# Optimization experiments

Measured on AMD Instinct MI355X. Metric: run time of the kernel, lower is better.

Reference implementation:

```python
import jax, jax.numpy as jnp
import numpy as np

N_HEADS = 16
N_UNITS = 1024
D_K = N_UNITS // N_HEADS
B, S = 2, 2048


def setup_inputs() -> dict:
    key = jax.random.key(0)
    ks = jax.random.split(key, 12)
    bound = 1.0 / np.sqrt(N_UNITS)
    u = lambda k, shape: jax.random.uniform(k, shape, jnp.float32, -bound, bound)
    inp = {
        'query': jax.random.normal(ks[0], (B, S, N_UNITS), jnp.float32),
        'key_': jax.random.normal(ks[1], (B, S, N_UNITS), jnp.float32),
        'value': jax.random.normal(ks[2], (B, S, N_UNITS), jnp.float32),
        'mask': jnp.broadcast_to(jnp.tril(jnp.ones((S, S), jnp.int32)), (B, S, S)),
        'Wq': u(ks[3], (N_UNITS, N_UNITS)), 'bq': u(ks[4], (N_UNITS,)),
        'Wk': u(ks[5], (N_UNITS, N_UNITS)), 'bk': u(ks[6], (N_UNITS,)),
        'Wv': u(ks[7], (N_UNITS, N_UNITS)), 'bv': u(ks[8], (N_UNITS,)),
        'Wo': u(ks[9], (N_UNITS, N_UNITS)), 'bo': u(ks[10], (N_UNITS,)),
    }
    return inp


def _split_heads(x):
    # [B,S,U] -> [B,H,S,Dk]
    b, s, _ = x.shape
    return x.reshape(b, s, N_HEADS, D_K).transpose(0, 2, 1, 3)


def reference(query, key_, value, mask, Wq, bq, Wk, bk, Wv, bv, Wo, bo):
    q = _split_heads(query @ Wq.T + bq)
    k = _split_heads(key_ @ Wk.T + bk)
    v = _split_heads(value @ Wv.T + bv)
    scores = jnp.einsum('bhqd,bhkd->bhqk', q, k) / jnp.sqrt(jnp.float32(D_K))
    scores = jnp.where(mask[:, None, :, :] == 0, jnp.float32(-1e10), scores)
    attn = jax.nn.softmax(scores, axis=-1)  # dropout omitted (eval / p=0)
    A = jnp.einsum('bhqk,bhkd->bhqd', attn, v)
    A = A.transpose(0, 2, 1, 3).reshape(query.shape[0], -1, N_UNITS)
    return A @ Wo.T + bo
```

## Files before the change

### kernel.cpp

```cpp
#include <hip/hip_runtime.h>
#include <hip/hip_bf16.h>

#define U     1024
#define SLEN  2048
#define HEADS 16
#define DK    64
#define MTOT  4096
#define MU    (MTOT * U)
#define UU    (U * U)

#define QSCALE2 0.18033688f

typedef unsigned short u16;
typedef short bf16x8 __attribute__((ext_vector_type(8)));
typedef u16 u16x4 __attribute__((ext_vector_type(4)));
typedef float f32x4 __attribute__((ext_vector_type(4)));

__device__ __forceinline__ u16 f2bf(float x) {
  union { float f; unsigned int u; } v; v.f = x;
  unsigned int r = v.u + 0x7fffu + ((v.u >> 16) & 1u);
  return (u16)(r >> 16);
}
__device__ __forceinline__ u16 f2bf_rz(float x) {
  return (u16)(__builtin_bit_cast(unsigned int, x) >> 16);
}

#if __has_builtin(__builtin_amdgcn_exp2f)
__device__ __forceinline__ float exp2_fast(float x) { return __builtin_amdgcn_exp2f(x); }
#else
__device__ __forceinline__ float exp2_fast(float x) { return __expf(x * 0.6931472f); }
#endif

__device__ __forceinline__ void async16(const u16* g, u16* lds) {
  __builtin_amdgcn_global_load_lds((const __attribute__((address_space(1))) void*)g,
                                   (__attribute__((address_space(3))) void*)lds,
                                   16, 0, 0);
}

#define DPP_F(x, ctrl) __builtin_bit_cast(float, \
    __builtin_amdgcn_update_dpp(0, __builtin_bit_cast(int, (x)), (ctrl), 0xF, 0xF, true))

__device__ __forceinline__ float rsum16(float x) {
  x += DPP_F(x, 0xB1);
  x += DPP_F(x, 0x4E);
  x += DPP_F(x, 0x141);
  x += DPP_F(x, 0x140);
  return x;
}

__global__ __launch_bounds__(256) void convert_kernel(
    const float* __restrict__ q, const float* __restrict__ k, const float* __restrict__ v,
    const float* __restrict__ wq, const float* __restrict__ wk,
    const float* __restrict__ wv, const float* __restrict__ wo,
    u16* __restrict__ cq, u16* __restrict__ ck, u16* __restrict__ cv,
    u16* __restrict__ cwq, u16* __restrict__ cwk, u16* __restrict__ cwv,
    u16* __restrict__ cwo) {
  const int t = blockIdx.y;
  const float* src = (t == 0) ? q : (t == 1) ? k : (t == 2) ? v
                   : (t == 3) ? wq : (t == 4) ? wk : (t == 5) ? wv : wo;
  u16* dst = (t == 0) ? cq : (t == 1) ? ck : (t == 2) ? cv
           : (t == 3) ? cwq : (t == 4) ? cwk : (t == 5) ? cwv : cwo;
  const int n4 = ((t < 3) ? MU : UU) >> 2;
  const int stride = gridDim.x * blockDim.x;
  for (int i = blockIdx.x * blockDim.x + threadIdx.x; i < n4; i += stride) {
    float4 f = ((const float4*)src)[i];
    u16x4 o = {f2bf(f.x), f2bf(f.y), f2bf(f.z), f2bf(f.w)};
    ((u16x4*)dst)[i] = o;
  }
}

__device__ __forceinline__ void stage_tile(const u16* __restrict__ src, int kt,
                                           u16* lds, int tid) {
#pragma unroll
  for (int c = 0; c < 2; ++c) {
    int f = c * 256 + tid;
    int row = f >> 2;
    int qs = f & 3;
    int q = qs ^ ((row >> 1) & 3);
    const u16* g = src + (size_t)row * U + kt + q * 8;
    u16* l = lds + (size_t)(f & ~63) * 8;
    async16(g, l);
  }
}

__device__ __forceinline__ bf16x8 read_frag(const u16* lds, int lrow, int quad) {
  int qs = quad ^ ((lrow >> 1) & 3);
  return *(const bf16x8*)(lds + (size_t)(lrow * 4 + qs) * 8);
}

__device__ __forceinline__ void gemm128(const u16* __restrict__ X,
                                        const u16* __restrict__ W,
                                        int m0, int n0, int tid,
                                        u16* lds,
                                        f32x4 acc[4][4]) {
  const int l = tid & 63, w = tid >> 6;
  const int quad = l >> 4, l15 = l & 15;
  const int wm = w & 1, wn = w >> 1;
  const u16* Xb = X + (size_t)m0 * U;
  const u16* Wb = W + (size_t)n0 * U;

  stage_tile(Xb, 0, lds, tid);
  stage_tile(Wb, 0, lds + 4096, tid);

  int bufsel = 0;
  for (int kt = 0; kt < U; kt += 32) {
    const int nxt = (bufsel == 2) ? 0 : bufsel + 1;
    if (kt + 32 < U) {
      stage_tile(Xb, kt + 32, lds + nxt * 8192, tid);
      stage_tile(Wb, kt + 32, lds + nxt * 8192 + 4096, tid);
      __builtin_amdgcn_sched_barrier(0);
      asm volatile("s_waitcnt vmcnt(4)" ::: "memory");
    } else {
      __builtin_amdgcn_sched_barrier(0);
      asm volatile("s_waitcnt vmcnt(0)" ::: "memory");
    }
    __builtin_amdgcn_sched_barrier(0);
    __builtin_amdgcn_s_barrier();
    __builtin_amdgcn_sched_barrier(0);

    const u16* la = lds + bufsel * 8192;
    const u16* lb = la + 4096;
    bf16x8 af[4], bfm[4];
#pragma unroll
    for (int i = 0; i < 4; ++i) af[i] = read_frag(la, wm * 64 + i * 16 + l15, quad);
#pragma unroll
    for (int t = 0; t < 4; ++t) bfm[t] = read_frag(lb, wn * 64 + t * 16 + l15, quad);
#pragma unroll
    for (int i = 0; i < 4; ++i)
#pragma unroll
      for (int t = 0; t < 4; ++t)
        acc[i][t] = __builtin_amdgcn_mfma_f32_16x16x32_bf16(af[i], bfm[t], acc[i][t], 0, 0, 0);
    bufsel = nxt;
  }
}

__device__ __forceinline__ void xcd_remap(int* m0, int* n0) {
  const int id = blockIdx.x + (blockIdx.y << 3);
  const int k = id & 7, j = id >> 3;
  const int xp = j >> 2;
  const int yp = (k << 2) | (j & 3);
  *m0 = yp * 128;
  *n0 = xp * 128;
}

__global__ __launch_bounds__(256) void qkv_gemm(
    const u16* __restrict__ q_in, const u16* __restrict__ k_in, const u16* __restrict__ v_in,
    const u16* __restrict__ Wq, const u16* __restrict__ Wk, const u16* __restrict__ Wv,
    const float* __restrict__ bq, const float* __restrict__ bk, const float* __restrict__ bv,
    u16* __restrict__ q_ws, u16* __restrict__ k_ws, u16* __restrict__ v_ws) {
  __shared__ __align__(16) u16 lds3[3 * 8192];
  const int z = blockIdx.z;
  const u16* X = (z == 0) ? q_in : (z == 1) ? k_in : v_in;
  const u16* W = (z == 0) ? Wq : (z == 1) ? Wk : Wv;
  const float* bias = (z == 0) ? bq : (z == 1) ? bk : bv;
  int m0, n0;
  xcd_remap(&m0, &n0);
  const int tid = threadIdx.x;
  f32x4 acc[4][4];
#pragma unroll
  for (int i = 0; i < 4; ++i)
#pragma unroll
    for (int t = 0; t < 4; ++t) acc[i][t] = (f32x4){0.f, 0.f, 0.f, 0.f};
  gemm128(X, W, m0, n0, tid, lds3, acc);

  const int l = tid & 63, w = tid >> 6;
  const int quad = l >> 4, l15 = l & 15;
  const int wm = w & 1, wn = w >> 1;
  const float osc = (z == 0) ? QSCALE2 : 1.0f;
#pragma unroll
  for (int t = 0; t < 4; ++t) {
    const int n = n0 + wn * 64 + t * 16 + l15;
    const float bb = bias[n];
    const int h = n >> 6, d = n & 63;
#pragma unroll
    for (int i = 0; i < 4; ++i) {
#pragma unroll
      for (int r = 0; r < 4; ++r) {
        const int m = m0 + wm * 64 + i * 16 + quad * 4 + r;
        const int b = m >> 11, s = m & (SLEN - 1);
        const int bh = b * HEADS + h;
        const u16 ov = f2bf((acc[i][t][r] + bb) * osc);
        if (z == 0)      q_ws[((size_t)bh * SLEN + s) * DK + d] = ov;
        else if (z == 1) k_ws[((size_t)bh * SLEN + s) * DK + d] = ov;
        else             v_ws[((size_t)bh * DK + d) * SLEN + s] = ov;
      }
    }
  }
}

__global__ __launch_bounds__(256, 4) void flash_attn(const u16* __restrict__ q_ws,
                                                     const u16* __restrict__ k_ws,
                                                     const u16* __restrict__ v_ws,
                                                     u16* __restrict__ a_ws) {
  __shared__ __align__(16) u16 kbuf[2][4096];
  __shared__ __align__(16) u16 vbuf[2][4096];
  __shared__ __align__(16) u16 p_lds[4][16][72];
  const int id = blockIdx.x;
  const int bh = id & 31;
  const int qblk = 31 - (id >> 5);
  const int tid = threadIdx.x;
  const int w = tid >> 6, l = tid & 63;
  const int quad = l >> 4, l15 = l & 15;
  const int qrow = qblk * 64 + w * 16;
  const int jn = qblk;

  const u16* qb = q_ws + (size_t)bh * SLEN * DK;
  const u16* kb = k_ws + (size_t)bh * SLEN * DK;
  const u16* vb = v_ws + (size_t)bh * DK * SLEN;

  bf16x8 aq0 = *(const bf16x8*)(qb + (size_t)(qrow + l15) * DK + quad * 8);
  bf16x8 aq1 = *(const bf16x8*)(qb + (size_t)(qrow + l15) * DK + 32 + quad * 8);

  f32x4 o[4];
  float l_run[4];
#pragma unroll
  for (int t = 0; t < 4; ++t) o[t] = (f32x4){0.f, 0.f, 0.f, 0.f};
#pragma unroll
  for (int r = 0; r < 4; ++r) l_run[r] = 0.f;

  auto stage = [&](int j0, int b) {
#pragma unroll
    for (int c = 0; c < 2; ++c) {
      const int f = c * 256 + tid;
      const int row = f >> 3, qs = f & 7;
      const int q = qs ^ (row & 7);
      u16* kdst = kbuf[b] + (size_t)(f & ~63) * 8;
      u16* vdst = vbuf[b] + (size_t)(f & ~63) * 8;
      async16(kb + (size_t)(j0 + row) * DK + q * 8, kdst);
      async16(vb + (size_t)row * SLEN + j0 + q * 8, vdst);
    }
  };

  stage(0, 0);
  __syncthreads();

  for (int jt = 0; jt <= jn; ++jt) {
    const int buf = jt & 1;
    if (jt < jn) stage((jt + 1) * 64, buf ^ 1);
    const int j0 = jt * 64;
    const int swz = l15 & 7;

    float sv[4][4];
#pragma unroll
    for (int t = 0; t < 4; ++t) {
      const u16* krow = kbuf[buf] + (size_t)(t * 16 + l15) * 64;
      bf16x8 kf0 = *(const bf16x8*)(krow + ((quad ^ swz) * 8));
      bf16x8 kf1 = *(const bf16x8*)(krow + (((quad + 4) ^ swz) * 8));
      f32x4 acc = (f32x4){0.f, 0.f, 0.f, 0.f};
      acc = __builtin_amdgcn_mfma_f32_16x16x32_bf16(aq0, kf0, acc, 0, 0, 0);
      acc = __builtin_amdgcn_mfma_f32_16x16x32_bf16(aq1, kf1, acc, 0, 0, 0);
#pragma unroll
      for (int r = 0; r < 4; ++r) sv[t][r] = acc[r];
    }
    if (jt == jn) {
#pragma unroll
      for (int t = 0; t < 4; ++t) {
        const int col = j0 + t * 16 + l15;
#pragma unroll
        for (int r = 0; r < 4; ++r)
          if (col > qrow + quad * 4 + r) sv[t][r] = -1e30f;
      }
    }
#pragma unroll
    for (int t = 0; t < 4; ++t) {
#pragma unroll
      for (int r = 0; r < 4; ++r) {
        const float p = exp2_fast(sv[t][r]);
        l_run[r] += p;
        p_lds[w][quad * 4 + r][t * 16 + l15] = f2bf_rz(p);
      }
    }
    bf16x8 pa0 = *(const bf16x8*)&p_lds[w][l15][quad * 8];
    bf16x8 pa1 = *(const bf16x8*)&p_lds[w][l15][32 + quad * 8];
#pragma unroll
    for (int t = 0; t < 4; ++t) {
      const u16* vrow = vbuf[buf] + (size_t)(t * 16 + l15) * 64;
      bf16x8 vf0 = *(const bf16x8*)(vrow + ((quad ^ swz) * 8));
      bf16x8 vf1 = *(const bf16x8*)(vrow + (((quad + 4) ^ swz) * 8));
      o[t] = __builtin_amdgcn_mfma_f32_16x16x32_bf16(pa0, vf0, o[t], 0, 0, 0);
      o[t] = __builtin_amdgcn_mfma_f32_16x16x32_bf16(pa1, vf1, o[t], 0, 0, 0);
    }
    __syncthreads();
  }
  const int b = bh >> 4, h = bh & 15;
  float inv[4];
#pragma unroll
  for (int r = 0; r < 4; ++r) inv[r] = 1.f / rsum16(l_run[r]);
#pragma unroll
  for (int r = 0; r < 4; ++r) {
    const int s = qrow + quad * 4 + r;
    u16* orow = a_ws + ((size_t)b * SLEN + s) * U + h * DK;
#pragma unroll
    for (int t = 0; t < 4; ++t)
      orow[t * 16 + l15] = f2bf(o[t][r] * inv[r]);
  }
}

__global__ __launch_bounds__(256) void oproj_gemm(const u16* __restrict__ A,
                                                  const u16* __restrict__ Wo,
                                                  const float* __restrict__ bo,
                                                  float* __restrict__ out) {
  __shared__ __align__(16) u16 lds3[3 * 8192];
  int m0, n0;
  xcd_remap(&m0, &n0);
  const int tid = threadIdx.x;
  f32x4 acc[4][4];
#pragma unroll
  for (int i = 0; i < 4; ++i)
#pragma unroll
    for (int t = 0; t < 4; ++t) acc[i][t] = (f32x4){0.f, 0.f, 0.f, 0.f};
  gemm128(A, Wo, m0, n0, tid, lds3, acc);

  const int l = tid & 63, w = tid >> 6;
  const int quad = l >> 4, l15 = l & 15;
  const int wm = w & 1, wn = w >> 1;
#pragma unroll
  for (int t = 0; t < 4; ++t) {
    const int n = n0 + wn * 64 + t * 16 + l15;
    const float bb = bo[n];
#pragma unroll
    for (int i = 0; i < 4; ++i) {
#pragma unroll
      for (int r = 0; r < 4; ++r) {
        const int m = m0 + wm * 64 + i * 16 + quad * 4 + r;
        out[(size_t)m * U + n] = acc[i][t][r] + bb;
      }
    }
  }
}

extern "C" void kernel_launch(void* const* d_in, const int* in_sizes, int n_in,
                              void* d_out, int out_size, void* d_ws, size_t ws_size,
                              hipStream_t stream) {
  (void)in_sizes; (void)n_in; (void)out_size; (void)ws_size;
  const float* query = (const float*)d_in[0];
  const float* key_  = (const float*)d_in[1];
  const float* value = (const float*)d_in[2];
  const float* Wq = (const float*)d_in[4];
  const float* bq = (const float*)d_in[5];
  const float* Wk = (const float*)d_in[6];
  const float* bk = (const float*)d_in[7];
  const float* Wv = (const float*)d_in[8];
  const float* bv = (const float*)d_in[9];
  const float* Wo = (const float*)d_in[10];
  const float* bo = (const float*)d_in[11];

  u16* ws = (u16*)d_ws;
  u16* cq  = ws;
  u16* ck  = cq + MU;
  u16* cv  = ck + MU;
  u16* cwq = cv + MU;
  u16* cwk = cwq + UU;
  u16* cwv = cwk + UU;
  u16* cwo = cwv + UU;
  u16* q_ws = cwo + UU;
  u16* k_ws = q_ws + MU;
  u16* v_ws = k_ws + MU;
  u16* a_ws = v_ws + MU;
  float* out = (float*)d_out;

  convert_kernel<<<dim3(512, 7), 256, 0, stream>>>(query, key_, value, Wq, Wk, Wv, Wo,
                                                   cq, ck, cv, cwq, cwk, cwv, cwo);
  qkv_gemm<<<dim3(8, 32, 3), 256, 0, stream>>>(cq, ck, cv, cwq, cwk, cwv,
                                               bq, bk, bv, q_ws, k_ws, v_ws);
  flash_attn<<<dim3(1024), 256, 0, stream>>>(q_ws, k_ws, v_ws, a_ws);
  oproj_gemm<<<dim3(8, 32), 256, 0, stream>>>(a_ws, cwo, bo, out);
}
```

Before: 230.7 us.

## Replace QKV GEMM with 256x256-tile, 512-thread, triple-buffered kernel

The 128x128 QKV projection kernel (768 blocks of 256 threads) is replaced by a 256x256-tile kernel using 512 threads, 96KB of dynamic LDS and a three-stage async load pipeline. The MFMA work is split into two halves separated by barriers, with s_setprio raising priority during math. A custom block-to-tile mapping spreads the 192 tiles across XCDs. The larger tiles raise operand reuse and cut global traffic, at the cost of fewer blocks (192 across 256 CUs), which leaves some CUs idle and adds more register pressure.

```diff
diff --git a/kernel.cpp b/kernel.cpp
--- a/kernel.cpp
+++ b/kernel.cpp
@@ -69,6 +69,124 @@
   }
 }
 
+__device__ __forceinline__ bf16x8 read_frag(const u16* lds, int lrow, int quad) {
+  int qs = quad ^ ((lrow >> 1) & 3);
+  return *(const bf16x8*)(lds + (size_t)(lrow * 4 + qs) * 8);
+}
+
+__global__ __launch_bounds__(512, 2) void qkv_gemm256(
+    const u16* __restrict__ q_in, const u16* __restrict__ k_in, const u16* __restrict__ v_in,
+    const u16* __restrict__ Wq, const u16* __restrict__ Wk, const u16* __restrict__ Wv,
+    const float* __restrict__ bq, const float* __restrict__ bk, const float* __restrict__ bv,
+    u16* __restrict__ q_ws, u16* __restrict__ k_ws, u16* __restrict__ v_ws) {
+  extern __shared__ __align__(16) u16 lds[];
+  const int id = blockIdx.x;
+  const int k8 = id & 7, j = id >> 3;
+  const int jm = j / 3, jn = j - jm * 3;
+  const int mp = (k8 & 1) * 8 + jm;
+  const int np = (k8 >> 1) * 3 + jn;
+  const int z = np >> 2;
+  const int m0 = mp * 256, n0 = (np & 3) * 256;
+  const u16* X = (z == 0) ? q_in : (z == 1) ? k_in : v_in;
+  const u16* W = (z == 0) ? Wq : (z == 1) ? Wk : Wv;
+  const float* bias = (z == 0) ? bq : (z == 1) ? bk : bv;
+  const u16* Xb = X + (size_t)m0 * U;
+  const u16* Wb = W + (size_t)n0 * U;
+
+  const int tid = threadIdx.x;
+  const int l = tid & 63, w = tid >> 6;
+  const int quad = l >> 4, l15 = l & 15;
+  const int wm = w & 1, wn = w >> 1;
+
+  auto stage = [&](const u16* src, int kt, u16* slot) {
+#pragma unroll
+    for (int L = 0; L < 2; ++L) {
+      const int f = L * 512 + tid;
+      const int row = f >> 2, qs = f & 3;
+      const int q = qs ^ ((row >> 1) & 3);
+      async16(src + (size_t)row * U + kt + q * 8, slot + (size_t)(f & ~63) * 8);
+    }
+  };
+
+  f32x4 acc[8][4];
+#pragma unroll
+  for (int i = 0; i < 8; ++i)
+#pragma unroll
+    for (int n = 0; n < 4; ++n) acc[i][n] = (f32x4){0.f, 0.f, 0.f, 0.f};
+
+  stage(Xb, 0, lds);
+  stage(Wb, 0, lds + 8192);
+  stage(Xb, 32, lds + 16384);
+  stage(Wb, 32, lds + 16384 + 8192);
+  __builtin_amdgcn_sched_barrier(0);
+  asm volatile("s_waitcnt vmcnt(4)" ::: "memory");
+  __builtin_amdgcn_s_barrier();
+
+  int scur = 0;
+  for (int t = 0; t < 32; ++t) {
+    u16* slot = lds + scur * 16384;
+    int s2 = scur + 2; if (s2 >= 3) s2 -= 3;
+    u16* slot2 = lds + s2 * 16384;
+    const int kt2 = (t + 2) * 32;
+    bf16x8 af[4], bf[4];
+#pragma unroll
+    for (int i = 0; i < 4; ++i) af[i] = read_frag(slot, wm * 128 + i * 16 + l15, quad);
+#pragma unroll
+    for (int n = 0; n < 4; ++n) bf[n] = read_frag(slot + 8192, wn * 64 + n * 16 + l15, quad);
+    if (t < 30) stage(Xb, kt2, slot2);
+    __builtin_amdgcn_s_barrier();
+    __builtin_amdgcn_s_setprio(1);
+#pragma unroll
+    for (int i = 0; i < 4; ++i)
+#pragma unroll
+      for (int n = 0; n < 4; ++n)
+        acc[i][n] = __builtin_amdgcn_mfma_f32_16x16x32_bf16(af[i], bf[n], acc[i][n], 0, 0, 0);
+    __builtin_amdgcn_s_setprio(0);
+    __builtin_amdgcn_s_barrier();
+#pragma unroll
+    for (int i = 0; i < 4; ++i) af[i] = read_frag(slot, wm * 128 + (4 + i) * 16 + l15, quad);
+    if (t < 30) {
+      stage(Wb, kt2, slot2 + 8192);
+      __builtin_amdgcn_sched_barrier(0);
+      asm volatile("s_waitcnt vmcnt(4)" ::: "memory");
+    } else {
+      __builtin_amdgcn_sched_barrier(0);
+      asm volatile("s_waitcnt vmcnt(0)" ::: "memory");
+    }
+    __builtin_amdgcn_s_barrier();
+    __builtin_amdgcn_s_setprio(1);
+#pragma unroll
+    for (int i = 0; i < 4; ++i)
+#pragma unroll
+      for (int n = 0; n < 4; ++n)
+        acc[4 + i][n] = __builtin_amdgcn_mfma_f32_16x16x32_bf16(af[i], bf[n], acc[4 + i][n], 0, 0, 0);
+    __builtin_amdgcn_s_setprio(0);
+    __builtin_amdgcn_s_barrier();
+    scur = (scur == 2) ? 0 : scur + 1;
+  }
+
+  const float osc = (z == 0) ? QSCALE2 : 1.0f;
+#pragma unroll
+  for (int nf = 0; nf < 4; ++nf) {
+    const int n = n0 + wn * 64 + nf * 16 + l15;
+    const float bb = bias[n];
+    const int h = n >> 6, d = n & 63;
+#pragma unroll
+    for (int mi = 0; mi < 8; ++mi) {
+#pragma unroll
+      for (int r = 0; r < 4; ++r) {
+        const int m = m0 + wm * 128 + mi * 16 + quad * 4 + r;
+        const int b = m >> 11, s = m & (SLEN - 1);
+        const int bh = b * HEADS + h;
+        const u16 ov = f2bf((acc[mi][nf][r] + bb) * osc);
+        if (z == 0)      q_ws[((size_t)bh * SLEN + s) * DK + d] = ov;
+        else if (z == 1) k_ws[((size_t)bh * SLEN + s) * DK + d] = ov;
+        else             v_ws[((size_t)bh * DK + d) * SLEN + s] = ov;
+      }
+    }
+  }
+}
+
 __device__ __forceinline__ void stage_tile(const u16* __restrict__ src, int kt,
                                            u16* lds, int tid) {
 #pragma unroll
@@ -81,11 +199,6 @@
     u16* l = lds + (size_t)(f & ~63) * 8;
     async16(g, l);
   }
-}
-
-__device__ __forceinline__ bf16x8 read_frag(const u16* lds, int lrow, int quad) {
-  int qs = quad ^ ((lrow >> 1) & 3);
-  return *(const bf16x8*)(lds + (size_t)(lrow * 4 + qs) * 8);
 }
 
 __device__ __forceinline__ void gemm128(const u16* __restrict__ X,
@@ -141,51 +254,6 @@
   const int yp = (k << 2) | (j & 3);
   *m0 = yp * 128;
   *n0 = xp * 128;
-}
-
-__global__ __launch_bounds__(256) void qkv_gemm(
-    const u16* __restrict__ q_in, const u16* __restrict__ k_in, const u16* __restrict__ v_in,
-    const u16* __restrict__ Wq, const u16* __restrict__ Wk, const u16* __restrict__ Wv,
-    const float* __restrict__ bq, const float* __restrict__ bk, const float* __restrict__ bv,
-    u16* __restrict__ q_ws, u16* __restrict__ k_ws, u16* __restrict__ v_ws) {
-  __shared__ __align__(16) u16 lds3[3 * 8192];
-  const int z = blockIdx.z;
-  const u16* X = (z == 0) ? q_in : (z == 1) ? k_in : v_in;
-  const u16* W = (z == 0) ? Wq : (z == 1) ? Wk : Wv;
-  const float* bias = (z == 0) ? bq : (z == 1) ? bk : bv;
-  int m0, n0;
-  xcd_remap(&m0, &n0);
-  const int tid = threadIdx.x;
-  f32x4 acc[4][4];
-#pragma unroll
-  for (int i = 0; i < 4; ++i)
-#pragma unroll
-    for (int t = 0; t < 4; ++t) acc[i][t] = (f32x4){0.f, 0.f, 0.f, 0.f};
-  gemm128(X, W, m0, n0, tid, lds3, acc);
-
-  const int l = tid & 63, w = tid >> 6;
-  const int quad = l >> 4, l15 = l & 15;
-  const int wm = w & 1, wn = w >> 1;
-  const float osc = (z == 0) ? QSCALE2 : 1.0f;
-#pragma unroll
-  for (int t = 0; t < 4; ++t) {
-    const int n = n0 + wn * 64 + t * 16 + l15;
-    const float bb = bias[n];
-    const int h = n >> 6, d = n & 63;
-#pragma unroll
-    for (int i = 0; i < 4; ++i) {
-#pragma unroll
-      for (int r = 0; r < 4; ++r) {
-        const int m = m0 + wm * 64 + i * 16 + quad * 4 + r;
-        const int b = m >> 11, s = m & (SLEN - 1);
-        const int bh = b * HEADS + h;
-        const u16 ov = f2bf((acc[i][t][r] + bb) * osc);
-        if (z == 0)      q_ws[((size_t)bh * SLEN + s) * DK + d] = ov;
-        else if (z == 1) k_ws[((size_t)bh * SLEN + s) * DK + d] = ov;
-        else             v_ws[((size_t)bh * DK + d) * SLEN + s] = ov;
-      }
-    }
-  }
 }
 
 __global__ __launch_bounds__(256, 4) void flash_attn(const u16* __restrict__ q_ws,
@@ -359,10 +427,13 @@
   u16* a_ws = v_ws + MU;
   float* out = (float*)d_out;
 
+  (void)hipFuncSetAttribute((const void*)qkv_gemm256,
+                            hipFuncAttributeMaxDynamicSharedMemorySize, 98304);
+
   convert_kernel<<<dim3(512, 7), 256, 0, stream>>>(query, key_, value, Wq, Wk, Wv, Wo,
                                                    cq, ck, cv, cwq, cwk, cwv, cwo);
-  qkv_gemm<<<dim3(8, 32, 3), 256, 0, stream>>>(cq, ck, cv, cwq, cwk, cwv,
-                                               bq, bk, bv, q_ws, k_ws, v_ws);
+  qkv_gemm256<<<dim3(192), 512, 98304, stream>>>(cq, ck, cv, cwq, cwk, cwv,
+                                                 bq, bk, bv, q_ws, k_ws, v_ws);
   flash_attn<<<dim3(1024), 256, 0, stream>>>(q_ws, k_ws, v_ws, a_ws);
   oproj_gemm<<<dim3(8, 32), 256, 0, stream>>>(a_ws, cwo, bo, out);
 }
```

After: 250.7 us. +8.7%, slower.

## Give each attention wave two 16-row query groups, halving block size

Applied to the files above, without the earlier changes.

The flash attention kernel now runs 2 waves per block instead of 4, and each wave handles 32 query rows as two 16-row groups. Every K and V fragment read from LDS is therefore reused for two MFMAs, which cuts LDS read traffic per unit of compute. The cost is more registers per wave (two sets of accumulators, Q fragments and scores) and fewer threads to stage K/V tiles. That could lower occupancy and leave less parallelism for hiding latency.

```diff
diff --git a/kernel.cpp b/kernel.cpp
--- a/kernel.cpp
+++ b/kernel.cpp
@@ -188,40 +188,47 @@
   }
 }
 
-__global__ __launch_bounds__(256, 4) void flash_attn(const u16* __restrict__ q_ws,
+__global__ __launch_bounds__(128, 3) void flash_attn(const u16* __restrict__ q_ws,
                                                      const u16* __restrict__ k_ws,
                                                      const u16* __restrict__ v_ws,
                                                      u16* __restrict__ a_ws) {
   __shared__ __align__(16) u16 kbuf[2][4096];
   __shared__ __align__(16) u16 vbuf[2][4096];
-  __shared__ __align__(16) u16 p_lds[4][16][72];
+  __shared__ __align__(16) u16 p_lds[2][32][72];
   const int id = blockIdx.x;
   const int bh = id & 31;
   const int qblk = 31 - (id >> 5);
   const int tid = threadIdx.x;
   const int w = tid >> 6, l = tid & 63;
   const int quad = l >> 4, l15 = l & 15;
-  const int qrow = qblk * 64 + w * 16;
+  const int qrow = qblk * 64 + w * 32;
   const int jn = qblk;
 
   const u16* qb = q_ws + (size_t)bh * SLEN * DK;
   const u16* kb = k_ws + (size_t)bh * SLEN * DK;
   const u16* vb = v_ws + (size_t)bh * DK * SLEN;
 
-  bf16x8 aq0 = *(const bf16x8*)(qb + (size_t)(qrow + l15) * DK + quad * 8);
-  bf16x8 aq1 = *(const bf16x8*)(qb + (size_t)(qrow + l15) * DK + 32 + quad * 8);
-
-  f32x4 o[4];
-  float l_run[4];
-#pragma unroll
-  for (int t = 0; t < 4; ++t) o[t] = (f32x4){0.f, 0.f, 0.f, 0.f};
-#pragma unroll
-  for (int r = 0; r < 4; ++r) l_run[r] = 0.f;
+  bf16x8 aq0[2], aq1[2];
+#pragma unroll
+  for (int g = 0; g < 2; ++g) {
+    aq0[g] = *(const bf16x8*)(qb + (size_t)(qrow + g * 16 + l15) * DK + quad * 8);
+    aq1[g] = *(const bf16x8*)(qb + (size_t)(qrow + g * 16 + l15) * DK + 32 + quad * 8);
+  }
+
+  f32x4 o[2][4];
+  float l_run[2][4];
+#pragma unroll
+  for (int g = 0; g < 2; ++g) {
+#pragma unroll
+    for (int t = 0; t < 4; ++t) o[g][t] = (f32x4){0.f, 0.f, 0.f, 0.f};
+#pragma unroll
+    for (int r = 0; r < 4; ++r) l_run[g][r] = 0.f;
+  }
 
   auto stage = [&](int j0, int b) {
 #pragma unroll
-    for (int c = 0; c < 2; ++c) {
-      const int f = c * 256 + tid;
+    for (int c = 0; c < 4; ++c) {
+      const int f = c * 128 + tid;
       const int row = f >> 3, qs = f & 7;
       const int q = qs ^ (row & 7);
       u16* kdst = kbuf[b] + (size_t)(f & ~63) * 8;
@@ -240,59 +247,76 @@
     const int j0 = jt * 64;
     const int swz = l15 & 7;
 
-    float sv[4][4];
+    float sv[2][4][4];
 #pragma unroll
     for (int t = 0; t < 4; ++t) {
       const u16* krow = kbuf[buf] + (size_t)(t * 16 + l15) * 64;
       bf16x8 kf0 = *(const bf16x8*)(krow + ((quad ^ swz) * 8));
       bf16x8 kf1 = *(const bf16x8*)(krow + (((quad + 4) ^ swz) * 8));
-      f32x4 acc = (f32x4){0.f, 0.f, 0.f, 0.f};
-      acc = __builtin_amdgcn_mfma_f32_16x16x32_bf16(aq0, kf0, acc, 0, 0, 0);
-      acc = __builtin_amdgcn_mfma_f32_16x16x32_bf16(aq1, kf1, acc, 0, 0, 0);
-#pragma unroll
-      for (int r = 0; r < 4; ++r) sv[t][r] = acc[r];
+#pragma unroll
+      for (int g = 0; g < 2; ++g) {
+        f32x4 acc = (f32x4){0.f, 0.f, 0.f, 0.f};
+        acc = __builtin_amdgcn_mfma_f32_16x16x32_bf16(aq0[g], kf0, acc, 0, 0, 0);
+        acc = __builtin_amdgcn_mfma_f32_16x16x32_bf16(aq1[g], kf1, acc, 0, 0, 0);
+#pragma unroll
+        for (int r = 0; r < 4; ++r) sv[g][t][r] = acc[r];
+      }
     }
     if (jt == jn) {
 #pragma unroll
+      for (int g = 0; g < 2; ++g)
+#pragma unroll
+        for (int t = 0; t < 4; ++t) {
+          const int col = j0 + t * 16 + l15;
+#pragma unroll
+          for (int r = 0; r < 4; ++r)
+            if (col > qrow + g * 16 + quad * 4 + r) sv[g][t][r] = -1e30f;
+        }
+    }
+#pragma unroll
+    for (int g = 0; g < 2; ++g)
+#pragma unroll
       for (int t = 0; t < 4; ++t) {
-        const int col = j0 + t * 16 + l15;
-#pragma unroll
-        for (int r = 0; r < 4; ++r)
-          if (col > qrow + quad * 4 + r) sv[t][r] = -1e30f;
-      }
-    }
-#pragma unroll
-    for (int t = 0; t < 4; ++t) {
-#pragma unroll
-      for (int r = 0; r < 4; ++r) {
-        const float p = exp2_fast(sv[t][r]);
-        l_run[r] += p;
-        p_lds[w][quad * 4 + r][t * 16 + l15] = f2bf_rz(p);
-      }
-    }
-    bf16x8 pa0 = *(const bf16x8*)&p_lds[w][l15][quad * 8];
-    bf16x8 pa1 = *(const bf16x8*)&p_lds[w][l15][32 + quad * 8];
+#pragma unroll
+        for (int r = 0; r < 4; ++r) {
+          const float p = exp2_fast(sv[g][t][r]);
+          l_run[g][r] += p;
+          p_lds[w][g * 16 + quad * 4 + r][t * 16 + l15] = f2bf_rz(p);
+        }
+      }
+    bf16x8 pa0[2], pa1[2];
+#pragma unroll
+    for (int g = 0; g < 2; ++g) {
+      pa0[g] = *(const bf16x8*)&p_lds[w][g * 16 + l15][quad * 8];
+      pa1[g] = *(const bf16x8*)&p_lds[w][g * 16 + l15][32 + quad * 8];
+    }
 #pragma unroll
     for (int t = 0; t < 4; ++t) {
       const u16* vrow = vbuf[buf] + (size_t)(t * 16 + l15) * 64;
       bf16x8 vf0 = *(const bf16x8*)(vrow + ((quad ^ swz) * 8));
       bf16x8 vf1 = *(const bf16x8*)(vrow + (((quad + 4) ^ swz) * 8));
-      o[t] = __builtin_amdgcn_mfma_f32_16x16x32_bf16(pa0, vf0, o[t], 0, 0, 0);
-      o[t] = __builtin_amdgcn_mfma_f32_16x16x32_bf16(pa1, vf1, o[t], 0, 0, 0);
+#pragma unroll
+      for (int g = 0; g < 2; ++g) {
+        o[g][t] = __builtin_amdgcn_mfma_f32_16x16x32_bf16(pa0[g], vf0, o[g][t], 0, 0, 0);
+        o[g][t] = __builtin_amdgcn_mfma_f32_16x16x32_bf16(pa1[g], vf1, o[g][t], 0, 0, 0);
+      }
     }
     __syncthreads();
   }
   const int b = bh >> 4, h = bh & 15;
-  float inv[4];
-#pragma unroll
-  for (int r = 0; r < 4; ++r) inv[r] = 1.f / rsum16(l_run[r]);
-#pragma unroll
-  for (int r = 0; r < 4; ++r) {
-    const int s = qrow + quad * 4 + r;
-    u16* orow = a_ws + ((size_t)b * SLEN + s) * U + h * DK;
-#pragma unroll
-    for (int t = 0; t < 4; ++t)
-      orow[t * 16 + l15] = f2bf(o[t][r] * inv[r]);
+#pragma unroll
+  for (int g = 0; g < 2; ++g) {
+    float inv[4];
+#pragma unroll
+    for (int r = 0; r < 4; ++r) inv[r] = 1.f / rsum16(l_run[g][r]);
+#pragma unroll
+    for (int r = 0; r < 4; ++r) {
+      const int s = qrow + g * 16 + quad * 4 + r;
+      u16* orow = a_ws + ((size_t)b * SLEN + s) * U + h * DK;
+#pragma unroll
+      for (int t = 0; t < 4; ++t)
+        orow[t * 16 + l15] = f2bf(o[g][t][r] * inv[r]);
+    }
   }
 }
 
@@ -363,6 +387,6 @@
                                                    cq, ck, cv, cwq, cwk, cwv, cwo);
   qkv_gemm<<<dim3(8, 32, 3), 256, 0, stream>>>(cq, ck, cv, cwq, cwk, cwv,
                                                bq, bk, bv, q_ws, k_ws, v_ws);
-  flash_attn<<<dim3(1024), 256, 0, stream>>>(q_ws, k_ws, v_ws, a_ws);
+  flash_attn<<<dim3(1024), 128, 0, stream>>>(q_ws, k_ws, v_ws, a_ws);
   oproj_gemm<<<dim3(8, 32), 256, 0, stream>>>(a_ws, cwo, bo, out);
 }
```

New measurement: 238.5 us. +3.4%, slower.
